# Kernel optimization log

Measured on AMD Instinct MI355X. Metric: run time of the kernel, lower is better.

## Reference

```python
import jax, jax.numpy as jnp
import numpy as np
from jax import lax

N_QUBITS = 8
N_LAYERS = 7


def _conv(x, w, b, stride, pad):
    y = lax.conv_general_dilated(x, w, (stride, stride), [(pad, pad), (pad, pad)],
                                 dimension_numbers=('NCHW', 'OIHW', 'NCHW'))
    return y + b[None, :, None, None]


def _apply_1q(psi, M, q):
    # psi: (B, 2,2,...,2); apply 2x2 real matrix M on qubit q (axis q+1)
    a = q + 1
    pm = jnp.moveaxis(psi, a, 1)
    out = jnp.einsum('ij,bj...->bi...', M, pm)
    return jnp.moveaxis(out, 1, a)


def _apply_cnot(psi, c, t):
    ac, at = c + 1, t + 1
    pm = jnp.moveaxis(psi, (ac, at), (1, 2))
    top = pm[:, 0]
    bot = jnp.flip(pm[:, 1], axis=1)  # flip target when control=1
    pm = jnp.stack([top, bot], axis=1)
    return jnp.moveaxis(pm, (1, 2), (ac, at))


def _quantum(features, qw):
    psi = features / jnp.linalg.norm(features, axis=1, keepdims=True)
    B = psi.shape[0]
    psi = psi.reshape((B,) + (2,) * N_QUBITS)
    for l in range(N_LAYERS):
        for q in range(N_QUBITS):
            th = qw[l, q] / 2.0
            c, s = jnp.cos(th), jnp.sin(th)
            M = jnp.stack([jnp.stack([c, -s]), jnp.stack([s, c])])
            psi = _apply_1q(psi, M, q)
        for q in range(N_QUBITS - 1):
            psi = _apply_cnot(psi, q, q + 1)
    p = psi.reshape(B, 2, -1) ** 2
    return jnp.sum(p[:, 0], axis=1) - jnp.sum(p[:, 1], axis=1)  # <PauliZ(0)>


def setup_inputs() -> dict:
    key = jax.random.key(0)
    ks = jax.random.split(key, 20)
    def g(k, shape, fan_in):
        return jax.random.normal(k, shape, jnp.float32) * (1.0 / np.sqrt(fan_in))
    inp = {
        'x':  jax.random.normal(ks[0], (4096, 1, 64, 64), jnp.float32),
        'w1': g(ks[1], (4, 1, 5, 5), 25), 'b1': jnp.zeros((4,), jnp.float32),
        'w2': g(ks[2], (8, 4, 3, 3), 36), 'b2': jnp.zeros((8,), jnp.float32),
        'w3': g(ks[3], (16, 8, 3, 3), 72), 'b3': jnp.zeros((16,), jnp.float32),
        'wf': g(ks[4], (256, 64), 64), 'bf': jnp.zeros((256,), jnp.float32),
        'qw': jax.random.uniform(ks[5], (7, 8), jnp.float32, 0.0, 2 * np.pi),
        'wc1': g(ks[6], (200, 1), 1),   'bc1': jnp.zeros((200,), jnp.float32),
        'wc2': g(ks[7], (150, 200), 200), 'bc2': jnp.zeros((150,), jnp.float32),
        'wc3': g(ks[8], (100, 150), 150), 'bc3': jnp.zeros((100,), jnp.float32),
        'wc4': g(ks[9], (50, 100), 100),  'bc4': jnp.zeros((50,), jnp.float32),
        'wc5': g(ks[10], (1, 50), 50),    'bc5': jnp.zeros((1,), jnp.float32),
    }
    return inp


def reference(x, w1, b1, w2, b2, w3, b3, wf, bf, qw,
              wc1, bc1, wc2, bc2, wc3, bc3, wc4, bc4, wc5, bc5):
    # CNN feature extractor (dropout = identity at inference)
    h = jax.nn.relu(_conv(x, w1, b1, 2, 2))   # (B,4,32,32)
    h = jax.nn.relu(_conv(h, w2, b2, 2, 1))   # (B,8,16,16)
    h = jax.nn.relu(_conv(h, w3, b3, 1, 1))   # (B,16,16,16)
    B = h.shape[0]
    # AdaptiveAvgPool2d(2): 16x16 -> 2x2 via 8x8 non-overlapping means
    h = h.reshape(B, 16, 2, 8, 2, 8).mean(axis=(3, 5))  # (B,16,2,2)
    h = h.reshape(B, 64)
    feats = jax.nn.relu(h @ wf.T + bf)        # (B,256)
    # F.normalize(p=2, dim=1)
    feats = feats / jnp.maximum(jnp.linalg.norm(feats, axis=1, keepdims=True), 1e-12)
    # Batched 8-qubit statevector simulation (replaces per-sample Python loop)
    q = _quantum(feats, qw)[:, None]          # (B,1)
    # MLP classifier
    h = jax.nn.relu(q @ wc1.T + bc1)
    h = jax.nn.relu(h @ wc2.T + bc2)
    h = jax.nn.relu(h @ wc3.T + bc3)
    h = jax.nn.relu(h @ wc4.T + bc4)
    return jax.nn.sigmoid(h @ wc5.T + bc5)    # (B,1)
```

## Files before the change

kernel.cpp:

```cpp
#include <hip/hip_runtime.h>
#include <math.h>

__global__ __launch_bounds__(256, 4)
void convpool_kernel(const float* __restrict__ x,
                     const float* __restrict__ w1, const float* __restrict__ b1,
                     const float* __restrict__ w2, const float* __restrict__ b2,
                     const float* __restrict__ w3, const float* __restrict__ b3,
                     float* __restrict__ poolout)
{
    __shared__ __align__(16) float regA[4160];
    __shared__ __align__(16) float regB[4620];
    __shared__ __align__(16) float w3s[1168];
    const int tid = threadIdx.x;
    const int b   = blockIdx.x;

    {
        const float4* xv = (const float4*)(x + (size_t)b * 4096);
        #pragma unroll
        for (int j = 0; j < 4; j++) {
            int i4 = j * 256 + tid;
            float4 v = xv[i4];
            int r = i4 >> 4, c = (i4 & 15) * 4;
            float* p = regA + r * 65 + c;
            p[0] = v.x; p[1] = v.y; p[2] = v.z; p[3] = v.w;
        }
        for (int i = tid; i < 1168; i += 256) w3s[i] = (i < 1152) ? w3[i] : b3[i - 1152];
        for (int i = tid; i < 140; i += 256) { int oc = i / 35, c = i - oc * 35; regB[oc * 1155 + c] = 0.f; }
        for (int i = tid; i < 132; i += 256) { int oc = i / 33, r = i - oc * 33; regB[oc * 1155 + r * 35] = 0.f; }
    }
    __syncthreads();

    {
        const int oh = tid >> 3, ow0 = (tid & 7) * 4;
        float acc[4][4];
        #pragma unroll
        for (int oc = 0; oc < 4; oc++) {
            const float bv = b1[oc];
            #pragma unroll
            for (int j = 0; j < 4; j++) acc[oc][j] = bv;
        }
        const int c0 = ow0 * 2 - 2;
        #pragma unroll
        for (int kh = 0; kh < 5; kh++) {
            const int ih = oh * 2 - 2 + kh;
            const bool rv = (ih >= 0) && (ih < 64);
            float colv[11];
            #pragma unroll
            for (int cc = 0; cc < 11; cc++) {
                const int c = c0 + cc;
                colv[cc] = (rv && c >= 0 && c < 64) ? regA[ih * 65 + c] : 0.f;
            }
            #pragma unroll
            for (int kw = 0; kw < 5; kw++) {
                #pragma unroll
                for (int oc = 0; oc < 4; oc++) {
                    const float wv = w1[oc * 25 + kh * 5 + kw];
                    acc[oc][0] = fmaf(colv[0 + kw], wv, acc[oc][0]);
                    acc[oc][1] = fmaf(colv[2 + kw], wv, acc[oc][1]);
                    acc[oc][2] = fmaf(colv[4 + kw], wv, acc[oc][2]);
                    acc[oc][3] = fmaf(colv[6 + kw], wv, acc[oc][3]);
                }
            }
        }
        #pragma unroll
        for (int oc = 0; oc < 4; oc++) {
            float* o = regB + oc * 1155 + (oh + 1) * 35 + ow0 + 1;
            #pragma unroll
            for (int j = 0; j < 4; j++) o[j] = fmaxf(acc[oc][j], 0.f);
        }
    }
    __syncthreads();

    for (int i = tid; i < 576; i += 256) {
        const int ch = i / 72, j = i - ch * 72;
        if (j < 18)      regA[ch * 324 + j] = 0.f;
        else if (j < 36) regA[ch * 324 + 17 * 18 + (j - 18)] = 0.f;
        else if (j < 52) regA[ch * 324 + (j - 35) * 18] = 0.f;
        else if (j < 68) regA[ch * 324 + (j - 51) * 18 + 17] = 0.f;
    }
    {
        const int lane = tid & 63;
        const int oc0  = __builtin_amdgcn_readfirstlane(tid >> 6);
        const int oh = lane >> 2, ow0 = (lane & 3) * 4;
        float acc[2][4];
        {
            const float ba = b2[oc0], bb = b2[oc0 + 4];
            #pragma unroll
            for (int j = 0; j < 4; j++) { acc[0][j] = ba; acc[1][j] = bb; }
        }
        const int c0s = ow0 * 2;
        #pragma unroll
        for (int ic = 0; ic < 4; ic++) {
            const float* base = regB + ic * 1155;
            #pragma unroll
            for (int kh = 0; kh < 3; kh++) {
                const int ihs = oh * 2 + kh;
                float colv[9];
                #pragma unroll
                for (int cc = 0; cc < 9; cc++) colv[cc] = base[ihs * 35 + c0s + cc];
                #pragma unroll
                for (int kw = 0; kw < 3; kw++) {
                    const float wa = w2[((oc0    ) * 4 + ic) * 9 + kh * 3 + kw];
                    const float wb = w2[((oc0 + 4) * 4 + ic) * 9 + kh * 3 + kw];
                    #pragma unroll
                    for (int j = 0; j < 4; j++) {
                        acc[0][j] = fmaf(colv[2 * j + kw], wa, acc[0][j]);
                        acc[1][j] = fmaf(colv[2 * j + kw], wb, acc[1][j]);
                    }
                }
            }
        }
        float* oA = regA + oc0 * 324       + (oh + 1) * 18 + ow0 + 1;
        float* oB = regA + (oc0 + 4) * 324 + (oh + 1) * 18 + ow0 + 1;
        #pragma unroll
        for (int j = 0; j < 4; j++) { oA[j] = fmaxf(acc[0][j], 0.f); oB[j] = fmaxf(acc[1][j], 0.f); }
    }
    __syncthreads();

    {
        const int oc = tid >> 4, s = tid & 15;
        const int tr = (s >> 2) * 4, tc = (s & 3) * 4;
        float acc[16];
        const float bv = w3s[1152 + oc];
        #pragma unroll
        for (int k = 0; k < 16; k++) acc[k] = bv;
        #pragma unroll
        for (int ic = 0; ic < 8; ic++) {
            const float* xc = regA + ic * 324;
            float p[6][6];
            #pragma unroll
            for (int dr = 0; dr < 6; dr++)
                #pragma unroll
                for (int dc = 0; dc < 6; dc++)
                    p[dr][dc] = xc[(tr + dr) * 18 + (tc + dc)];
            float wv[9];
            #pragma unroll
            for (int k = 0; k < 9; k++) wv[k] = w3s[oc * 72 + ic * 9 + k];
            #pragma unroll
            for (int r = 0; r < 4; r++)
                #pragma unroll
                for (int c = 0; c < 4; c++) {
                    float a = acc[r * 4 + c];
                    #pragma unroll
                    for (int kh = 0; kh < 3; kh++)
                        #pragma unroll
                        for (int kw = 0; kw < 3; kw++)
                            a = fmaf(p[r + kh][c + kw], wv[kh * 3 + kw], a);
                    acc[r * 4 + c] = a;
                }
        }
        float* o = regB + oc * 273;
        #pragma unroll
        for (int r = 0; r < 4; r++)
            #pragma unroll
            for (int c = 0; c < 4; c++)
                o[(tr + r) * 17 + tc + c] = fmaxf(acc[r * 4 + c], 0.f);
    }
    __syncthreads();

    if (tid < 64) {
        const int ch = tid >> 2, ii = (tid >> 1) & 1, jj = tid & 1;
        const float* p = regB + ch * 273 + (ii * 8) * 17 + jj * 8;
        float s = 0.f;
        #pragma unroll
        for (int hh = 0; hh < 8; hh++)
            #pragma unroll
            for (int ww = 0; ww < 8; ww++) s += p[hh * 17 + ww];
        poolout[b * 64 + tid] = s * (1.f / 64.f);
    }
}

__global__ __launch_bounds__(256)
void head_kernel(const float* __restrict__ poolin,
                 const float* __restrict__ wf, const float* __restrict__ bf,
                 const float* __restrict__ qw,
                 const float* __restrict__ wc1, const float* __restrict__ bc1,
                 const float* __restrict__ wc2, const float* __restrict__ bc2,
                 const float* __restrict__ wc3, const float* __restrict__ bc3,
                 const float* __restrict__ wc4, const float* __restrict__ bc4,
                 const float* __restrict__ wc5, const float* __restrict__ bc5,
                 float* __restrict__ out)
{
    __shared__ __align__(16) float pool_s[512];
    __shared__ __align__(16) float feats[2048];
    __shared__ __align__(16) float h1[1600];
    __shared__ __align__(16) float h2[1200];
    __shared__ __align__(16) float h3[800];
    __shared__ __align__(16) float h4[400];
    __shared__ float zbuf[8];
    __shared__ float csc[56], css[56];

    const int tid  = threadIdx.x;
    const int blk  = blockIdx.x;
    const int lane = tid & 63;
    const int wv   = tid >> 6;

    ((float2*)pool_s)[tid] = ((const float2*)(poolin + (size_t)blk * 512))[tid];
    if (tid < 56) {
        float th = qw[tid] * 0.5f;
        csc[tid] = cosf(th);
        css[tid] = sinf(th);
    }
    __syncthreads();

    {
        float acc[8];
        const float bv = bf[tid];
        #pragma unroll
        for (int e = 0; e < 8; e++) acc[e] = bv;
        const float4* wr = (const float4*)(wf + tid * 64);
        #pragma unroll
        for (int kc = 0; kc < 4; kc++) {
            float4 w0 = wr[kc * 4 + 0], w1_ = wr[kc * 4 + 1], w2_ = wr[kc * 4 + 2], w3_ = wr[kc * 4 + 3];
            #pragma unroll
            for (int e = 0; e < 8; e++) {
                const float4* pp = (const float4*)(pool_s + e * 64 + kc * 16);
                float4 p0 = pp[0], p1 = pp[1], p2 = pp[2], p3 = pp[3];
                float a = acc[e];
                a = fmaf(w0.x, p0.x, a); a = fmaf(w0.y, p0.y, a); a = fmaf(w0.z, p0.z, a); a = fmaf(w0.w, p0.w, a);
                a = fmaf(w1_.x, p1.x, a); a = fmaf(w1_.y, p1.y, a); a = fmaf(w1_.z, p1.z, a); a = fmaf(w1_.w, p1.w, a);
                a = fmaf(w2_.x, p2.x, a); a = fmaf(w2_.y, p2.y, a); a = fmaf(w2_.z, p2.z, a); a = fmaf(w2_.w, p2.w, a);
                a = fmaf(w3_.x, p3.x, a); a = fmaf(w3_.y, p3.y, a); a = fmaf(w3_.z, p3.z, a); a = fmaf(w3_.w, p3.w, a);
                acc[e] = a;
            }
        }
        #pragma unroll
        for (int e = 0; e < 8; e++) feats[e * 256 + tid] = fmaxf(acc[e], 0.f);
    }
    __syncthreads();

    {
        float v[2][4];
        #pragma unroll
        for (int u = 0; u < 2; u++) {
            const float* base = feats + (wv * 2 + u) * 256;
            v[u][0] = base[lane]; v[u][1] = base[64 + lane];
            v[u][2] = base[128 + lane]; v[u][3] = base[192 + lane];
        }
        float ssq[2];
        #pragma unroll
        for (int u = 0; u < 2; u++)
            ssq[u] = v[u][0]*v[u][0] + v[u][1]*v[u][1] + v[u][2]*v[u][2] + v[u][3]*v[u][3];
        #pragma unroll
        for (int off = 1; off < 64; off <<= 1) {
            ssq[0] += __shfl_xor(ssq[0], off, 64);
            ssq[1] += __shfl_xor(ssq[1], off, 64);
        }
        #pragma unroll
        for (int u = 0; u < 2; u++) {
            const float inv = 1.0f / fmaxf(sqrtf(ssq[u]), 1e-12f);
            v[u][0] *= inv; v[u][1] *= inv; v[u][2] *= inv; v[u][3] *= inv;
        }

        for (int l = 0; l < 7; l++) {
            #pragma unroll
            for (int u = 0; u < 2; u++) {
                float c = csc[l * 8 + 0], s = css[l * 8 + 0];
                float n0 = c*v[u][0] - s*v[u][2], n2 = s*v[u][0] + c*v[u][2];
                float n1 = c*v[u][1] - s*v[u][3], n3 = s*v[u][1] + c*v[u][3];
                float c1 = csc[l * 8 + 1], s1 = css[l * 8 + 1];
                v[u][0] = c1*n0 - s1*n1; v[u][1] = s1*n0 + c1*n1;
                v[u][2] = c1*n2 - s1*n3; v[u][3] = s1*n2 + c1*n3;
            }
            #pragma unroll
            for (int q = 2; q < 8; q++) {
                const int m = 1 << (7 - q);
                const float c = csc[l * 8 + q], s = css[l * 8 + q];
                const float sgn = (lane & m) ? s : -s;
                #pragma unroll
                for (int u = 0; u < 2; u++) {
                    float t0 = __shfl_xor(v[u][0], m, 64);
                    float t1 = __shfl_xor(v[u][1], m, 64);
                    float t2 = __shfl_xor(v[u][2], m, 64);
                    float t3 = __shfl_xor(v[u][3], m, 64);
                    v[u][0] = fmaf(sgn, t0, c * v[u][0]);
                    v[u][1] = fmaf(sgn, t1, c * v[u][1]);
                    v[u][2] = fmaf(sgn, t2, c * v[u][2]);
                    v[u][3] = fmaf(sgn, t3, c * v[u][3]);
                }
            }
            #pragma unroll
            for (int u = 0; u < 2; u++) {
                float t = v[u][2]; v[u][2] = v[u][3]; v[u][3] = t;
                v[u][1] = __shfl_xor(v[u][1], 32, 64);
                v[u][3] = __shfl_xor(v[u][3], 32, 64);
            }
            #pragma unroll
            for (int q = 2; q < 7; q++) {
                const int mc = 1 << (7 - q), mt = 1 << (6 - q);
                #pragma unroll
                for (int u = 0; u < 2; u++) {
                    float t0 = __shfl_xor(v[u][0], mt, 64);
                    float t1 = __shfl_xor(v[u][1], mt, 64);
                    float t2 = __shfl_xor(v[u][2], mt, 64);
                    float t3 = __shfl_xor(v[u][3], mt, 64);
                    if (lane & mc) { v[u][0] = t0; v[u][1] = t1; v[u][2] = t2; v[u][3] = t3; }
                }
            }
        }
        float m0[2];
        #pragma unroll
        for (int u = 0; u < 2; u++)
            m0[u] = v[u][0]*v[u][0] + v[u][1]*v[u][1] - v[u][2]*v[u][2] - v[u][3]*v[u][3];
        #pragma unroll
        for (int off = 1; off < 64; off <<= 1) {
            m0[0] += __shfl_xor(m0[0], off, 64);
            m0[1] += __shfl_xor(m0[1], off, 64);
        }
        if (lane == 0) { zbuf[wv * 2] = m0[0]; zbuf[wv * 2 + 1] = m0[1]; }
    }
    __syncthreads();

    if (tid < 200) {
        const float w = wc1[tid], bv = bc1[tid];
        #pragma unroll
        for (int e = 0; e < 8; e++) h1[e * 200 + tid] = fmaxf(fmaf(zbuf[e], w, bv), 0.f);
    }
    __syncthreads();
    if (tid < 150) {
        float acc[8];
        const float bv = bc2[tid];
        #pragma unroll
        for (int e = 0; e < 8; e++) acc[e] = bv;
        const float4* wr = (const float4*)(wc2 + tid * 200);
        for (int kc = 0; kc < 25; kc++) {
            float4 wa = wr[2 * kc], wb = wr[2 * kc + 1];
            #pragma unroll
            for (int e = 0; e < 8; e++) {
                const float4* hp = (const float4*)(h1 + e * 200) + 2 * kc;
                float4 ha = hp[0], hb = hp[1];
                float a = acc[e];
                a = fmaf(wa.x, ha.x, a); a = fmaf(wa.y, ha.y, a); a = fmaf(wa.z, ha.z, a); a = fmaf(wa.w, ha.w, a);
                a = fmaf(wb.x, hb.x, a); a = fmaf(wb.y, hb.y, a); a = fmaf(wb.z, hb.z, a); a = fmaf(wb.w, hb.w, a);
                acc[e] = a;
            }
        }
        #pragma unroll
        for (int e = 0; e < 8; e++) h2[e * 150 + tid] = fmaxf(acc[e], 0.f);
    }
    __syncthreads();
    if (tid < 100) {
        float acc[8];
        const float bv = bc3[tid];
        #pragma unroll
        for (int e = 0; e < 8; e++) acc[e] = bv;
        const float2* wr = (const float2*)(wc3 + tid * 150);
        for (int k = 0; k < 75; k++) {
            float2 wa = wr[k];
            #pragma unroll
            for (int e = 0; e < 8; e++) {
                float2 hv = ((const float2*)(h2 + e * 150))[k];
                acc[e] = fmaf(wa.x, hv.x, fmaf(wa.y, hv.y, acc[e]));
            }
        }
        #pragma unroll
        for (int e = 0; e < 8; e++) h3[e * 100 + tid] = fmaxf(acc[e], 0.f);
    }
    __syncthreads();
    if (tid < 50) {
        float acc[8];
        const float bv = bc4[tid];
        #pragma unroll
        for (int e = 0; e < 8; e++) acc[e] = bv;
        const float4* wr = (const float4*)(wc4 + tid * 100);
        for (int kc = 0; kc < 25; kc++) {
            float4 wa = wr[kc];
            #pragma unroll
            for (int e = 0; e < 8; e++) {
                float4 hv = ((const float4*)(h3 + e * 100))[kc];
                float a = acc[e];
                a = fmaf(wa.x, hv.x, a); a = fmaf(wa.y, hv.y, a);
                a = fmaf(wa.z, hv.z, a); a = fmaf(wa.w, hv.w, a);
                acc[e] = a;
            }
        }
        #pragma unroll
        for (int e = 0; e < 8; e++) h4[e * 50 + tid] = fmaxf(acc[e], 0.f);
    }
    __syncthreads();
    if (tid < 8) {
        float acc = bc5[0];
        const float2* wr = (const float2*)wc5;
        #pragma unroll
        for (int k = 0; k < 25; k++) {
            float2 wa = wr[k];
            float2 hv = ((const float2*)(h4 + tid * 50))[k];
            acc = fmaf(wa.x, hv.x, fmaf(wa.y, hv.y, acc));
        }
        out[blk * 8 + tid] = 1.0f / (1.0f + expf(-acc));
    }
}

extern "C" void kernel_launch(void* const* d_in, const int* in_sizes, int n_in,
                              void* d_out, int out_size, void* d_ws, size_t ws_size,
                              hipStream_t stream) {
    const float* x   = (const float*)d_in[0];
    const float* w1  = (const float*)d_in[1];
    const float* b1  = (const float*)d_in[2];
    const float* w2  = (const float*)d_in[3];
    const float* b2  = (const float*)d_in[4];
    const float* w3  = (const float*)d_in[5];
    const float* b3  = (const float*)d_in[6];
    const float* wf  = (const float*)d_in[7];
    const float* bf  = (const float*)d_in[8];
    const float* qw  = (const float*)d_in[9];
    const float* wc1 = (const float*)d_in[10];
    const float* bc1 = (const float*)d_in[11];
    const float* wc2 = (const float*)d_in[12];
    const float* bc2 = (const float*)d_in[13];
    const float* wc3 = (const float*)d_in[14];
    const float* bc3 = (const float*)d_in[15];
    const float* wc4 = (const float*)d_in[16];
    const float* bc4 = (const float*)d_in[17];
    const float* wc5 = (const float*)d_in[18];
    const float* bc5 = (const float*)d_in[19];
    float* out = (float*)d_out;

    float* poolbuf = (float*)d_ws;

    convpool_kernel<<<4096, 256, 0, stream>>>(x, w1, b1, w2, b2, w3, b3, poolbuf);
    head_kernel<<<512, 256, 0, stream>>>(poolbuf, wf, bf, qw,
                                         wc1, bc1, wc2, bc2, wc3, bc3,
                                         wc4, bc4, wc5, bc5, out);
}
```

Before: 234.4 us.

## Merge conv LDS buffers, read input from global, fuse pooling into conv3, halve head batch

The conv kernel drops the staged input tile and reads conv1 inputs straight from global memory. Its two LDS regions are merged into one arena, with conv2 results held in registers across an extra barrier so the arena can be reused. Conv3 now pools via wave shuffles instead of writing to LDS and reducing. Lower LDS use allows a 6-block launch bound. The head kernel processes 4 samples per block over twice as many blocks, one sample per wave, trading per-block reuse of weights for more parallelism.

```diff
diff --git a/kernel.cpp b/kernel.cpp
--- a/kernel.cpp
+++ b/kernel.cpp
@@ -1,37 +1,31 @@
 #include <hip/hip_runtime.h>
 #include <math.h>
 
-__global__ __launch_bounds__(256, 4)
+__global__ __launch_bounds__(256, 6)
 void convpool_kernel(const float* __restrict__ x,
                      const float* __restrict__ w1, const float* __restrict__ b1,
                      const float* __restrict__ w2, const float* __restrict__ b2,
                      const float* __restrict__ w3, const float* __restrict__ b3,
                      float* __restrict__ poolout)
 {
-    __shared__ __align__(16) float regA[4160];
-    __shared__ __align__(16) float regB[4620];
+    __shared__ __align__(16) float arena[4620];
     __shared__ __align__(16) float w3s[1168];
-    const int tid = threadIdx.x;
-    const int b   = blockIdx.x;
-
-    {
-        const float4* xv = (const float4*)(x + (size_t)b * 4096);
-        #pragma unroll
-        for (int j = 0; j < 4; j++) {
-            int i4 = j * 256 + tid;
-            float4 v = xv[i4];
-            int r = i4 >> 4, c = (i4 & 15) * 4;
-            float* p = regA + r * 65 + c;
-            p[0] = v.x; p[1] = v.y; p[2] = v.z; p[3] = v.w;
-        }
-        for (int i = tid; i < 1168; i += 256) w3s[i] = (i < 1152) ? w3[i] : b3[i - 1152];
-        for (int i = tid; i < 140; i += 256) { int oc = i / 35, c = i - oc * 35; regB[oc * 1155 + c] = 0.f; }
-        for (int i = tid; i < 132; i += 256) { int oc = i / 33, r = i - oc * 33; regB[oc * 1155 + r * 35] = 0.f; }
-    }
-    __syncthreads();
-
-    {
-        const int oh = tid >> 3, ow0 = (tid & 7) * 4;
+    const int tid  = threadIdx.x;
+    const int b    = blockIdx.x;
+    const int lane = tid & 63;
+
+    for (int i = tid; i < 1168; i += 256) w3s[i] = (i < 1152) ? w3[i] : b3[i - 1152];
+    for (int i = tid; i < 140; i += 256) { int oc = i / 35, c = i - oc * 35; arena[oc * 1155 + c] = 0.f; }
+    for (int i = tid; i < 132; i += 256) { int oc = i / 33, r = i - oc * 33; arena[oc * 1155 + r * 35] = 0.f; }
+
+    {
+        const float* xb = x + (size_t)b * 4096;
+        const int oh  = tid >> 3;
+        const int ow  = tid & 7;
+        const int ow0 = ow * 4;
+        const int c0  = ow0 * 2 - 2;
+        const bool cmL = (ow == 0);
+        const bool cmR = (ow == 7);
         float acc[4][4];
         #pragma unroll
         for (int oc = 0; oc < 4; oc++) {
@@ -39,59 +33,57 @@
             #pragma unroll
             for (int j = 0; j < 4; j++) acc[oc][j] = bv;
         }
-        const int c0 = ow0 * 2 - 2;
         #pragma unroll
         for (int kh = 0; kh < 5; kh++) {
             const int ih = oh * 2 - 2 + kh;
-            const bool rv = (ih >= 0) && (ih < 64);
-            float colv[11];
-            #pragma unroll
-            for (int cc = 0; cc < 11; cc++) {
-                const int c = c0 + cc;
-                colv[cc] = (rv && c >= 0 && c < 64) ? regA[ih * 65 + c] : 0.f;
-            }
-            #pragma unroll
-            for (int kw = 0; kw < 5; kw++) {
-                #pragma unroll
-                for (int oc = 0; oc < 4; oc++) {
-                    const float wv = w1[oc * 25 + kh * 5 + kw];
-                    acc[oc][0] = fmaf(colv[0 + kw], wv, acc[oc][0]);
-                    acc[oc][1] = fmaf(colv[2 + kw], wv, acc[oc][1]);
-                    acc[oc][2] = fmaf(colv[4 + kw], wv, acc[oc][2]);
-                    acc[oc][3] = fmaf(colv[6 + kw], wv, acc[oc][3]);
+            if (ih >= 0 && ih < 64) {
+                const float* row = xb + ih * 64;
+                float colv[11];
+                {
+                    float v0 = row[cmL ? 0 : c0];
+                    float v1 = row[cmL ? 0 : c0 + 1];
+                    float vA = row[cmR ? 63 : c0 + 10];
+                    colv[0]  = cmL ? 0.f : v0;
+                    colv[1]  = cmL ? 0.f : v1;
+                    colv[10] = cmR ? 0.f : vA;
                 }
+                #pragma unroll
+                for (int cc = 2; cc < 10; cc++) colv[cc] = row[c0 + cc];
+                #pragma unroll
+                for (int kw = 0; kw < 5; kw++) {
+                    #pragma unroll
+                    for (int oc = 0; oc < 4; oc++) {
+                        const float wv = w1[oc * 25 + kh * 5 + kw];
+                        acc[oc][0] = fmaf(colv[0 + kw], wv, acc[oc][0]);
+                        acc[oc][1] = fmaf(colv[2 + kw], wv, acc[oc][1]);
+                        acc[oc][2] = fmaf(colv[4 + kw], wv, acc[oc][2]);
+                        acc[oc][3] = fmaf(colv[6 + kw], wv, acc[oc][3]);
+                    }
+                }
             }
         }
         #pragma unroll
         for (int oc = 0; oc < 4; oc++) {
-            float* o = regB + oc * 1155 + (oh + 1) * 35 + ow0 + 1;
+            float* o = arena + oc * 1155 + (oh + 1) * 35 + ow0 + 1;
             #pragma unroll
             for (int j = 0; j < 4; j++) o[j] = fmaxf(acc[oc][j], 0.f);
         }
     }
     __syncthreads();
 
-    for (int i = tid; i < 576; i += 256) {
-        const int ch = i / 72, j = i - ch * 72;
-        if (j < 18)      regA[ch * 324 + j] = 0.f;
-        else if (j < 36) regA[ch * 324 + 17 * 18 + (j - 18)] = 0.f;
-        else if (j < 52) regA[ch * 324 + (j - 35) * 18] = 0.f;
-        else if (j < 68) regA[ch * 324 + (j - 51) * 18 + 17] = 0.f;
-    }
-    {
-        const int lane = tid & 63;
-        const int oc0  = __builtin_amdgcn_readfirstlane(tid >> 6);
-        const int oh = lane >> 2, ow0 = (lane & 3) * 4;
-        float acc[2][4];
+    float r2[2][4];
+    {
+        const int oc0 = __builtin_amdgcn_readfirstlane(tid >> 6);
+        const int oh  = lane >> 2, ow0 = (lane & 3) * 4;
         {
             const float ba = b2[oc0], bb = b2[oc0 + 4];
             #pragma unroll
-            for (int j = 0; j < 4; j++) { acc[0][j] = ba; acc[1][j] = bb; }
+            for (int j = 0; j < 4; j++) { r2[0][j] = ba; r2[1][j] = bb; }
         }
         const int c0s = ow0 * 2;
         #pragma unroll
         for (int ic = 0; ic < 4; ic++) {
-            const float* base = regB + ic * 1155;
+            const float* base = arena + ic * 1155;
             #pragma unroll
             for (int kh = 0; kh < 3; kh++) {
                 const int ihs = oh * 2 + kh;
@@ -104,16 +96,29 @@
                     const float wb = w2[((oc0 + 4) * 4 + ic) * 9 + kh * 3 + kw];
                     #pragma unroll
                     for (int j = 0; j < 4; j++) {
-                        acc[0][j] = fmaf(colv[2 * j + kw], wa, acc[0][j]);
-                        acc[1][j] = fmaf(colv[2 * j + kw], wb, acc[1][j]);
+                        r2[0][j] = fmaf(colv[2 * j + kw], wa, r2[0][j]);
+                        r2[1][j] = fmaf(colv[2 * j + kw], wb, r2[1][j]);
                     }
                 }
             }
         }
-        float* oA = regA + oc0 * 324       + (oh + 1) * 18 + ow0 + 1;
-        float* oB = regA + (oc0 + 4) * 324 + (oh + 1) * 18 + ow0 + 1;
-        #pragma unroll
-        for (int j = 0; j < 4; j++) { oA[j] = fmaxf(acc[0][j], 0.f); oB[j] = fmaxf(acc[1][j], 0.f); }
+    }
+    __syncthreads();
+
+    for (int i = tid; i < 576; i += 256) {
+        const int ch = i / 72, j = i - ch * 72;
+        if (j < 18)      arena[ch * 324 + j] = 0.f;
+        else if (j < 36) arena[ch * 324 + 17 * 18 + (j - 18)] = 0.f;
+        else if (j < 52) arena[ch * 324 + (j - 35) * 18] = 0.f;
+        else if (j < 68) arena[ch * 324 + (j - 51) * 18 + 17] = 0.f;
+    }
+    {
+        const int oc0 = __builtin_amdgcn_readfirstlane(tid >> 6);
+        const int oh  = lane >> 2, ow0 = (lane & 3) * 4;
+        float* oA = arena + oc0 * 324       + (oh + 1) * 18 + ow0 + 1;
+        float* oB = arena + (oc0 + 4) * 324 + (oh + 1) * 18 + ow0 + 1;
+        #pragma unroll
+        for (int j = 0; j < 4; j++) { oA[j] = fmaxf(r2[0][j], 0.f); oB[j] = fmaxf(r2[1][j], 0.f); }
     }
     __syncthreads();
 
@@ -126,7 +131,7 @@
         for (int k = 0; k < 16; k++) acc[k] = bv;
         #pragma unroll
         for (int ic = 0; ic < 8; ic++) {
-            const float* xc = regA + ic * 324;
+            const float* xc = arena + ic * 324;
             float p[6][6];
             #pragma unroll
             for (int dr = 0; dr < 6; dr++)
@@ -149,24 +154,15 @@
                     acc[r * 4 + c] = a;
                 }
         }
-        float* o = regB + oc * 273;
-        #pragma unroll
-        for (int r = 0; r < 4; r++)
-            #pragma unroll
-            for (int c = 0; c < 4; c++)
-                o[(tr + r) * 17 + tc + c] = fmaxf(acc[r * 4 + c], 0.f);
-    }
-    __syncthreads();
-
-    if (tid < 64) {
-        const int ch = tid >> 2, ii = (tid >> 1) & 1, jj = tid & 1;
-        const float* p = regB + ch * 273 + (ii * 8) * 17 + jj * 8;
-        float s = 0.f;
-        #pragma unroll
-        for (int hh = 0; hh < 8; hh++)
-            #pragma unroll
-            for (int ww = 0; ww < 8; ww++) s += p[hh * 17 + ww];
-        poolout[b * 64 + tid] = s * (1.f / 64.f);
+        float ps = 0.f;
+        #pragma unroll
+        for (int k = 0; k < 16; k++) ps += fmaxf(acc[k], 0.f);
+        ps += __shfl_xor(ps, 1, 64);
+        ps += __shfl_xor(ps, 4, 64);
+        if ((s & 5) == 0) {
+            const int ii = s >> 3, jj = (s >> 1) & 1;
+            poolout[b * 64 + oc * 4 + ii * 2 + jj] = ps * (1.f / 64.f);
+        }
     }
 }
 
@@ -181,13 +177,13 @@
                  const float* __restrict__ wc5, const float* __restrict__ bc5,
                  float* __restrict__ out)
 {
-    __shared__ __align__(16) float pool_s[512];
-    __shared__ __align__(16) float feats[2048];
-    __shared__ __align__(16) float h1[1600];
-    __shared__ __align__(16) float h2[1200];
-    __shared__ __align__(16) float h3[800];
-    __shared__ __align__(16) float h4[400];
-    __shared__ float zbuf[8];
+    __shared__ __align__(16) float pool_s[256];
+    __shared__ __align__(16) float feats[1024];
+    __shared__ __align__(16) float h1[800];
+    __shared__ __align__(16) float h2[600];
+    __shared__ __align__(16) float h3[400];
+    __shared__ __align__(16) float h4[200];
+    __shared__ float zbuf[4];
     __shared__ float csc[56], css[56];
 
     const int tid  = threadIdx.x;
@@ -195,7 +191,7 @@
     const int lane = tid & 63;
     const int wv   = tid >> 6;
 
-    ((float2*)pool_s)[tid] = ((const float2*)(poolin + (size_t)blk * 512))[tid];
+    pool_s[tid] = poolin[(size_t)blk * 256 + tid];
     if (tid < 56) {
         float th = qw[tid] * 0.5f;
         csc[tid] = cosf(th);
@@ -204,16 +200,16 @@
     __syncthreads();
 
     {
-        float acc[8];
+        float acc[4];
         const float bv = bf[tid];
         #pragma unroll
-        for (int e = 0; e < 8; e++) acc[e] = bv;
+        for (int e = 0; e < 4; e++) acc[e] = bv;
         const float4* wr = (const float4*)(wf + tid * 64);
         #pragma unroll
         for (int kc = 0; kc < 4; kc++) {
             float4 w0 = wr[kc * 4 + 0], w1_ = wr[kc * 4 + 1], w2_ = wr[kc * 4 + 2], w3_ = wr[kc * 4 + 3];
             #pragma unroll
-            for (int e = 0; e < 8; e++) {
+            for (int e = 0; e < 4; e++) {
                 const float4* pp = (const float4*)(pool_s + e * 64 + kc * 16);
                 float4 p0 = pp[0], p1 = pp[1], p2 = pp[2], p3 = pp[3];
                 float a = acc[e];
@@ -225,108 +221,79 @@
             }
         }
         #pragma unroll
-        for (int e = 0; e < 8; e++) feats[e * 256 + tid] = fmaxf(acc[e], 0.f);
-    }
-    __syncthreads();
-
-    {
-        float v[2][4];
-        #pragma unroll
-        for (int u = 0; u < 2; u++) {
-            const float* base = feats + (wv * 2 + u) * 256;
-            v[u][0] = base[lane]; v[u][1] = base[64 + lane];
-            v[u][2] = base[128 + lane]; v[u][3] = base[192 + lane];
-        }
-        float ssq[2];
-        #pragma unroll
-        for (int u = 0; u < 2; u++)
-            ssq[u] = v[u][0]*v[u][0] + v[u][1]*v[u][1] + v[u][2]*v[u][2] + v[u][3]*v[u][3];
-        #pragma unroll
-        for (int off = 1; off < 64; off <<= 1) {
-            ssq[0] += __shfl_xor(ssq[0], off, 64);
-            ssq[1] += __shfl_xor(ssq[1], off, 64);
-        }
-        #pragma unroll
-        for (int u = 0; u < 2; u++) {
-            const float inv = 1.0f / fmaxf(sqrtf(ssq[u]), 1e-12f);
-            v[u][0] *= inv; v[u][1] *= inv; v[u][2] *= inv; v[u][3] *= inv;
-        }
+        for (int e = 0; e < 4; e++) feats[e * 256 + tid] = fmaxf(acc[e], 0.f);
+    }
+    __syncthreads();
+
+    {
+        const float* base = feats + wv * 256;
+        float v0 = base[lane], v1 = base[64 + lane];
+        float v2 = base[128 + lane], v3 = base[192 + lane];
+        float ssq = v0 * v0 + v1 * v1 + v2 * v2 + v3 * v3;
+        #pragma unroll
+        for (int off = 1; off < 64; off <<= 1) ssq += __shfl_xor(ssq, off, 64);
+        const float inv = 1.0f / fmaxf(sqrtf(ssq), 1e-12f);
+        v0 *= inv; v1 *= inv; v2 *= inv; v3 *= inv;
 
         for (int l = 0; l < 7; l++) {
-            #pragma unroll
-            for (int u = 0; u < 2; u++) {
+            {
                 float c = csc[l * 8 + 0], s = css[l * 8 + 0];
-                float n0 = c*v[u][0] - s*v[u][2], n2 = s*v[u][0] + c*v[u][2];
-                float n1 = c*v[u][1] - s*v[u][3], n3 = s*v[u][1] + c*v[u][3];
+                float n0 = c * v0 - s * v2, n2 = s * v0 + c * v2;
+                float n1 = c * v1 - s * v3, n3 = s * v1 + c * v3;
                 float c1 = csc[l * 8 + 1], s1 = css[l * 8 + 1];
-                v[u][0] = c1*n0 - s1*n1; v[u][1] = s1*n0 + c1*n1;
-                v[u][2] = c1*n2 - s1*n3; v[u][3] = s1*n2 + c1*n3;
+                v0 = c1 * n0 - s1 * n1; v1 = s1 * n0 + c1 * n1;
+                v2 = c1 * n2 - s1 * n3; v3 = s1 * n2 + c1 * n3;
             }
             #pragma unroll
             for (int q = 2; q < 8; q++) {
                 const int m = 1 << (7 - q);
                 const float c = csc[l * 8 + q], s = css[l * 8 + q];
                 const float sgn = (lane & m) ? s : -s;
-                #pragma unroll
-                for (int u = 0; u < 2; u++) {
-                    float t0 = __shfl_xor(v[u][0], m, 64);
-                    float t1 = __shfl_xor(v[u][1], m, 64);
-                    float t2 = __shfl_xor(v[u][2], m, 64);
-                    float t3 = __shfl_xor(v[u][3], m, 64);
-                    v[u][0] = fmaf(sgn, t0, c * v[u][0]);
-                    v[u][1] = fmaf(sgn, t1, c * v[u][1]);
-                    v[u][2] = fmaf(sgn, t2, c * v[u][2]);
-                    v[u][3] = fmaf(sgn, t3, c * v[u][3]);
-                }
-            }
-            #pragma unroll
-            for (int u = 0; u < 2; u++) {
-                float t = v[u][2]; v[u][2] = v[u][3]; v[u][3] = t;
-                v[u][1] = __shfl_xor(v[u][1], 32, 64);
-                v[u][3] = __shfl_xor(v[u][3], 32, 64);
-            }
+                float t0 = __shfl_xor(v0, m, 64);
+                float t1 = __shfl_xor(v1, m, 64);
+                float t2 = __shfl_xor(v2, m, 64);
+                float t3 = __shfl_xor(v3, m, 64);
+                v0 = fmaf(sgn, t0, c * v0);
+                v1 = fmaf(sgn, t1, c * v1);
+                v2 = fmaf(sgn, t2, c * v2);
+                v3 = fmaf(sgn, t3, c * v3);
+            }
+            { float t = v2; v2 = v3; v3 = t; }
+            v1 = __shfl_xor(v1, 32, 64);
+            v3 = __shfl_xor(v3, 32, 64);
             #pragma unroll
             for (int q = 2; q < 7; q++) {
                 const int mc = 1 << (7 - q), mt = 1 << (6 - q);
-                #pragma unroll
-                for (int u = 0; u < 2; u++) {
-                    float t0 = __shfl_xor(v[u][0], mt, 64);
-                    float t1 = __shfl_xor(v[u][1], mt, 64);
-                    float t2 = __shfl_xor(v[u][2], mt, 64);
-                    float t3 = __shfl_xor(v[u][3], mt, 64);
-                    if (lane & mc) { v[u][0] = t0; v[u][1] = t1; v[u][2] = t2; v[u][3] = t3; }
-                }
-            }
-        }
-        float m0[2];
-        #pragma unroll
-        for (int u = 0; u < 2; u++)
-            m0[u] = v[u][0]*v[u][0] + v[u][1]*v[u][1] - v[u][2]*v[u][2] - v[u][3]*v[u][3];
-        #pragma unroll
-        for (int off = 1; off < 64; off <<= 1) {
-            m0[0] += __shfl_xor(m0[0], off, 64);
-            m0[1] += __shfl_xor(m0[1], off, 64);
-        }
-        if (lane == 0) { zbuf[wv * 2] = m0[0]; zbuf[wv * 2 + 1] = m0[1]; }
+                float t0 = __shfl_xor(v0, mt, 64);
+                float t1 = __shfl_xor(v1, mt, 64);
+                float t2 = __shfl_xor(v2, mt, 64);
+                float t3 = __shfl_xor(v3, mt, 64);
+                if (lane & mc) { v0 = t0; v1 = t1; v2 = t2; v3 = t3; }
+            }
+        }
+        float m0 = v0 * v0 + v1 * v1 - v2 * v2 - v3 * v3;
+        #pragma unroll
+        for (int off = 1; off < 64; off <<= 1) m0 += __shfl_xor(m0, off, 64);
+        if (lane == 0) zbuf[wv] = m0;
     }
     __syncthreads();
 
     if (tid < 200) {
         const float w = wc1[tid], bv = bc1[tid];
         #pragma unroll
-        for (int e = 0; e < 8; e++) h1[e * 200 + tid] = fmaxf(fmaf(zbuf[e], w, bv), 0.f);
+        for (int e = 0; e < 4; e++) h1[e * 200 + tid] = fmaxf(fmaf(zbuf[e], w, bv), 0.f);
     }
     __syncthreads();
     if (tid < 150) {
-        float acc[8];
+        float acc[4];
         const float bv = bc2[tid];
         #pragma unroll
-        for (int e = 0; e < 8; e++) acc[e] = bv;
+        for (int e = 0; e < 4; e++) acc[e] = bv;
         const float4* wr = (const float4*)(wc2 + tid * 200);
         for (int kc = 0; kc < 25; kc++) {
             float4 wa = wr[2 * kc], wb = wr[2 * kc + 1];
             #pragma unroll
-            for (int e = 0; e < 8; e++) {
+            for (int e = 0; e < 4; e++) {
                 const float4* hp = (const float4*)(h1 + e * 200) + 2 * kc;
                 float4 ha = hp[0], hb = hp[1];
                 float a = acc[e];
@@ -336,37 +303,37 @@
             }
         }
         #pragma unroll
-        for (int e = 0; e < 8; e++) h2[e * 150 + tid] = fmaxf(acc[e], 0.f);
+        for (int e = 0; e < 4; e++) h2[e * 150 + tid] = fmaxf(acc[e], 0.f);
     }
     __syncthreads();
     if (tid < 100) {
-        float acc[8];
+        float acc[4];
         const float bv = bc3[tid];
         #pragma unroll
-        for (int e = 0; e < 8; e++) acc[e] = bv;
+        for (int e = 0; e < 4; e++) acc[e] = bv;
         const float2* wr = (const float2*)(wc3 + tid * 150);
         for (int k = 0; k < 75; k++) {
             float2 wa = wr[k];
             #pragma unroll
-            for (int e = 0; e < 8; e++) {
+            for (int e = 0; e < 4; e++) {
                 float2 hv = ((const float2*)(h2 + e * 150))[k];
                 acc[e] = fmaf(wa.x, hv.x, fmaf(wa.y, hv.y, acc[e]));
             }
         }
         #pragma unroll
-        for (int e = 0; e < 8; e++) h3[e * 100 + tid] = fmaxf(acc[e], 0.f);
+        for (int e = 0; e < 4; e++) h3[e * 100 + tid] = fmaxf(acc[e], 0.f);
     }
     __syncthreads();
     if (tid < 50) {
-        float acc[8];
+        float acc[4];
         const float bv = bc4[tid];
         #pragma unroll
-        for (int e = 0; e < 8; e++) acc[e] = bv;
+        for (int e = 0; e < 4; e++) acc[e] = bv;
         const float4* wr = (const float4*)(wc4 + tid * 100);
         for (int kc = 0; kc < 25; kc++) {
             float4 wa = wr[kc];
             #pragma unroll
-            for (int e = 0; e < 8; e++) {
+            for (int e = 0; e < 4; e++) {
                 float4 hv = ((const float4*)(h3 + e * 100))[kc];
                 float a = acc[e];
                 a = fmaf(wa.x, hv.x, a); a = fmaf(wa.y, hv.y, a);
@@ -375,10 +342,10 @@
             }
         }
         #pragma unroll
-        for (int e = 0; e < 8; e++) h4[e * 50 + tid] = fmaxf(acc[e], 0.f);
-    }
-    __syncthreads();
-    if (tid < 8) {
+        for (int e = 0; e < 4; e++) h4[e * 50 + tid] = fmaxf(acc[e], 0.f);
+    }
+    __syncthreads();
+    if (tid < 4) {
         float acc = bc5[0];
         const float2* wr = (const float2*)wc5;
         #pragma unroll
@@ -387,7 +354,7 @@
             float2 hv = ((const float2*)(h4 + tid * 50))[k];
             acc = fmaf(wa.x, hv.x, fmaf(wa.y, hv.y, acc));
         }
-        out[blk * 8 + tid] = 1.0f / (1.0f + expf(-acc));
+        out[blk * 4 + tid] = 1.0f / (1.0f + expf(-acc));
     }
 }
 
@@ -419,7 +386,7 @@
     float* poolbuf = (float*)d_ws;
 
     convpool_kernel<<<4096, 256, 0, stream>>>(x, w1, b1, w2, b2, w3, b3, poolbuf);
-    head_kernel<<<512, 256, 0, stream>>>(poolbuf, wf, bf, qw,
-                                         wc1, bc1, wc2, bc2, wc3, bc3,
-                                         wc4, bc4, wc5, bc5, out);
+    head_kernel<<<1024, 256, 0, stream>>>(poolbuf, wf, bf, qw,
+                                          wc1, bc1, wc2, bc2, wc3, bc3,
+                                          wc4, bc4, wc5, bc5, out);
 }
```

New measurement: 218.5 us. 6.8% less time.
